# Kernel optimization log

Measured on AMD Instinct MI355X. Metric: run time of the kernel, lower is better.

## Reference

```python
import jax, jax.numpy as jnp
import numpy as np

SR = 22050
FLOOR = 60.0
BPO = 12

def _interp_linear(p, T):
    # torch F.interpolate(mode='linear', align_corners=False)
    S = p.shape[0]
    x = np.clip((np.arange(T, dtype=np.float64) + 0.5) * (S / T) - 0.5, 0.0, S - 1)
    i0 = np.floor(x).astype(np.int64)
    i1 = np.minimum(i0 + 1, S - 1)
    f = (x - i0).astype(np.float32)
    return p[i0] * (1.0 - f) + p[i1] * f

def _hann(n):
    # torch.hann_window(n, periodic=True)
    if n <= 0:
        return np.zeros((0,), np.float32)
    return (0.5 - 0.5 * np.cos(2.0 * np.pi * np.arange(n) / n)).astype(np.float32)

def _find_voiced(f0, i):
    sub = f0[i:]
    if sub.size == 0:
        return None
    flag = (sub > 0.0).astype(np.int64)
    flag[0] = 0
    if not flag.any():
        return None
    rel = int(flag.argmax())
    after = flag[rel:]
    z = np.nonzero(after == 0)[0]
    run = int(z[0]) if z.size else int(after.size)
    return i + rel, i + rel + run

def _l2n(v):
    # F.normalize(dim=-1), eps=1e-12
    return v / np.maximum(np.linalg.norm(v, axis=-1, keepdims=True), 1e-12)

def _find_peak(signal, f0, i, right_dir):
    w = int(SR / max(float(f0[i]), FLOOR))
    s = max(i - w // 2, 0)
    if right_dir:
        cand_l, cand_r = int(i + 0.3 * w), int(i + 0.75 * w)
    else:
        cand_l, cand_r = max(int(i - 1.75 * w), 0), max(int(i - 1.3 * w), 0)
    if cand_l == cand_r or len(signal) - cand_l < w:
        return w, -1.0, i, 0.0
    seg = np.lib.stride_tricks.sliding_window_view(signal[cand_l:cand_r + w], w)
    corr = _l2n(seg) @ _l2n(signal[s:s + w])
    r = int(corr.argmax())
    return w, float(corr[r]), i + (r + cand_l) - s, float(np.abs(seg[r]).max())

def _find_allpeaks(signal, f0):
    gp = float(np.abs(signal).max())
    added_right, i, peaks = -1e308, 0, []
    while True:
        voiced = _find_voiced(f0, i)
        if voiced is None:
            break
        left, right = voiced
        middle = (left + right) // 2
        w = int(SR / float(f0[middle]))
        s = max(middle - w // 2, 0)
        seg = signal[s:s + w]
        mn, imn = float(seg.min()), int(seg.argmin())
        mx, imx = float(seg.max()), int(seg.argmax())
        i = middle if mn == mx else s + (imn if abs(mn) > abs(mx) else imx)
        backup = i
        while True:
            w, corr, i, peak = _find_peak(signal, f0, i, False)
            if corr == -1.0:
                i -= w
            if i < left:
                if corr > 0.7 and peak > 0.023333 * gp and i - added_right > 0.8 * w:
                    peaks.append(i)
                break
            if corr > 0.3 and (peak == 0.0 or peak > 0.01 * gp):
                if i - added_right > 0.8 * w:
                    peaks.append(i)
        i = backup
        while True:
            w, corr, i, peak = _find_peak(signal, f0, i, True)
            if corr == -1.0:
                i += w
            if i >= right:
                if corr > 0.7 and peak > 0.023333 * gp:
                    peaks.append(i)
                    added_right = i
                break
            if corr > 0.3 and (peak == 0.0 or peak > 0.01 * gp):
                peaks.append(i)
                added_right = i
        i = right
    if not peaks:
        return None
    return np.clip(np.array(sorted(peaks), dtype=np.int64), 0, len(signal) - 1)

def _psola_plan(signal, pitch, peaks):
    # Returns list of (dst_idx, src_idx, window) overlap-add ops plus tail index.
    T = len(signal)
    idx = np.arange(T)
    max_w = 1.25 * SR / float(pitch[pitch > 0].min())
    ops, i = [], 0
    while i < T:
        voiced = _find_voiced(pitch, i)
        if voiced is None:
            break
        left_v, right_v = voiced
        if i < left_v:
            ops.append((idx[i:left_v], idx[i:left_v], _hann(left_v - i)))
        while left_v < right_v:
            p = int(np.abs(peaks - left_v).argmin())
            period = int(SR / max(float(pitch[left_v]), FLOOR))
            left_w = right_w = period // 2
            if p > 0 and peaks[p] - peaks[p - 1] <= max_w:
                left_w = min(int(peaks[p] - peaks[p - 1]), left_w)
            if p < len(peaks) - 1 and peaks[p + 1] - peaks[p] <= max_w:
                right_w = min(int(peaks[p + 1] - peaks[p]), right_w)
            left_i = max(int(peaks[p]) - left_w, 0)
            right_i = int(peaks[p]) + right_w
            ival = (right_i - left_i) // 2
            if ival <= 0:  # safety guard; unreachable for speech-range pitch
                break
            win = _hann(ival * 2)
            seglen = min(len(idx[left_v - ival:left_v + ival]), len(idx[left_i:left_i + ival * 2]))
            dst = idx[left_v - ival:left_v - ival + seglen]
            src = idx[left_i:left_i + seglen]
            L = min(len(dst), len(src), seglen)
            ops.append((dst[:L], src[:L], win[:L]))
            left_v += ival * 2
        i = right_v
    return ops, i

def _pitch_shift_plan(snd, pitch, steps, pitch_range):
    if not (pitch > 1e-05).any():
        return None
    f0 = _interp_linear(pitch, len(snd))
    peaks = _find_allpeaks(snd, f0)
    if peaks is None:
        return None
    v = np.sort(pitch[pitch > 0.0])
    median = float(v[(len(v) - 1) // 2])  # torch lower median
    factor = 2.0 ** (steps / BPO)
    f0, median = f0 * factor, median * factor
    f0 = np.where(f0 > 0.0, median + (f0 - median) * pitch_range, 0.0).astype(np.float32)
    return _psola_plan(snd, f0, peaks)

def setup_inputs():
    key = jax.random.key(0)
    T, S = 661500, 3000
    t = np.arange(S)
    base = (170.0 + 40.0 * np.sin(2.0 * np.pi * t / 400.0)).astype(np.float32)
    voiced = (t % 75) >= 15  # alternating unvoiced/voiced runs
    pitch = np.where(voiced, base, 0.0).astype(np.float32)
    f0 = _interp_linear(pitch, T)
    phase = 2.0 * np.pi * np.cumsum(f0.astype(np.float64)) / SR
    noise = np.asarray(jax.random.normal(key, (T,)), np.float32)
    snd = np.where(f0 > 0.0, 0.55 * np.sin(phase) + 0.25 * np.sin(2 * phase) + 0.1 * np.sin(3 * phase), 0.0)
    snd = np.clip(snd + 0.02 * noise, -1.0, 1.0).astype(np.float32)
    return {"snd": jnp.asarray(snd), "pitch": jnp.asarray(pitch), "steps": 3, "pitch_range": jnp.float32(1.0)}

def reference(snd, pitch, steps, pitch_range):
    snd_np = np.asarray(snd, np.float32)
    pitch_np = np.asarray(pitch, np.float32)
    plan = _pitch_shift_plan(snd_np, pitch_np, int(steps), float(pitch_range))
    if plan is None:
        return jnp.asarray(snd_np)
    ops, tail = plan
    out = np.zeros_like(snd_np)
    for dst, src, win in ops:
        out[dst] += win * snd_np[src]
    out[tail:] = snd_np[tail:]
    return jnp.asarray(out)
```

## Files before the change

kernel.cpp:

```cpp
#include <hip/hip_runtime.h>
#include <cfloat>
#include <climits>
#include <math.h>

#define SRATE 22050.0
#define WMAX 512
#define RCAP 128
#define LCR 256
#define RCR 512
#define SCAP 16384
#define OPR 256
#define MSL 3072
#define NTW 256
#define NTM 1024
#define PCAP 8192
#define FCAP 16384
#define PSTG 4096
#define SNDW 15872
#define RPW 136

__global__ __launch_bounds__(256) void kinit_stats(const float* __restrict__ pitch, int S, unsigned* scal) {
  __shared__ int sc[256];
  __shared__ int sa[256];
  int tid = threadIdx.x;
  if (tid < 64) scal[tid] = (tid == 1) ? 0x7f800000u : 0u;
  int c = 0, a = 0;
  for (int j = tid; j < S; j += 256) {
    float v = pitch[j];
    if (v > 0.0f) c++;
    if (v > 1e-05f) a = 1;
  }
  sc[tid] = c; sa[tid] = a; __syncthreads();
  for (int st = 128; st; st >>= 1) {
    if (tid < st) { sc[tid] += sc[tid + st]; sa[tid] |= sa[tid + st]; }
    __syncthreads();
  }
  if (tid == 0) { scal[15] = (unsigned)sc[0]; scal[3] = (unsigned)sa[0]; }
}

__global__ __launch_bounds__(256) void kmedsel(const float* __restrict__ pitch, int S, unsigned* scal) {
  __shared__ float sp[MSL];
  __shared__ unsigned hist[256];
  __shared__ unsigned sprefix, smask;
  __shared__ int srank;
  int tid = threadIdx.x;
  int n = (int)scal[15];
  if (n == 0) return;
  bool lds = (S <= MSL);
  if (lds) { for (int q = tid; q < S; q += 256) sp[q] = pitch[q]; }
  if (tid == 0) { sprefix = 0u; smask = 0u; srank = (n - 1) >> 1; }
  __syncthreads();
  for (int shift = 24; shift >= 0; shift -= 8) {
    hist[tid] = 0u;
    __syncthreads();
    unsigned pfx = sprefix, msk = smask;
    for (int q = tid; q < S; q += 256) {
      float v = lds ? sp[q] : pitch[q];
      if (v > 0.0f) {
        unsigned u = __float_as_uint(v);
        if ((u & msk) == pfx) atomicAdd(&hist[(u >> shift) & 255u], 1u);
      }
    }
    __syncthreads();
    if (tid == 0) {
      int r = srank;
      unsigned b = 0;
      for (;;) { unsigned cc = hist[b]; if (r < (int)cc) break; r -= (int)cc; b++; }
      srank = r;
      sprefix = pfx | (b << shift);
      smask = msk | (0xFFu << shift);
    }
    __syncthreads();
  }
  if (tid == 0) scal[2] = sprefix;
}

__device__ __forceinline__ float interp1(const float* __restrict__ pitch, int S, double r, int t) {
  double x = ((double)t + 0.5) * r - 0.5;
  if (x < 0.0) x = 0.0;
  double sm1 = (double)(S - 1);
  if (x > sm1) x = sm1;
  double fl = floor(x);
  int i0 = (int)fl;
  int i1 = i0 + 1; if (i1 > S - 1) i1 = S - 1;
  float f = (float)(x - fl);
  return __fadd_rn(__fmul_rn(pitch[i0], __fsub_rn(1.0f, f)), __fmul_rn(pitch[i1], f));
}

__global__ __launch_bounds__(256) void kprep(const float* __restrict__ pitch, int S, int T,
                                             const float* __restrict__ snd, unsigned* scal,
                                             const int* __restrict__ steps_p, const float* __restrict__ pr_p,
                                             float* __restrict__ f0, float* __restrict__ f0s,
                                             int* __restrict__ pd, int* __restrict__ w0,
                                             int* s0l, int* e0l, int* s1l, int* e1l) {
  __shared__ float smax[256];
  __shared__ unsigned smin[256];
  float med = __uint_as_float(scal[2]);
  double factor = exp2((double)steps_p[0] / 12.0);
  float fac32 = (float)factor;
  float m32 = (float)((double)med * factor);
  float pr32 = pr_p[0];
  double r = (double)S / (double)T;
  float amax = 0.0f;
  unsigned lmin = 0x7f800000u;
  int stride = gridDim.x * blockDim.x;
  for (int t = blockIdx.x * blockDim.x + threadIdx.x; t < T; t += stride) {
    float v = interp1(pitch, S, r, t);
    f0[t] = v;
    float v1 = __fmul_rn(v, fac32);
    float vs = 0.0f;
    if (v1 > 0.0f) vs = __fadd_rn(m32, __fmul_rn(__fsub_rn(v1, m32), pr32));
    f0s[t] = vs;
    { double fd = (double)vs; if (fd < 60.0) fd = 60.0; pd[t] = (int)(SRATE / fd); }
    { double fi = (double)v; if (fi < 60.0) fi = 60.0;
      int ww = (int)(SRATE / fi); if (ww < 1) ww = 1; if (ww > WMAX - 1) ww = WMAX - 1;
      w0[t] = ww; }
    if (vs > 0.0f) { unsigned b = __float_as_uint(vs); if (b < lmin) lmin = b; }
    float a = fabsf(snd[t]); if (a > amax) amax = a;
    bool pv = false, pv1 = false;
    if (t > 0) {
      float pvv = interp1(pitch, S, r, t - 1);
      pv = pvv > 0.0f;
      float pm1 = __fmul_rn(pvv, fac32);
      float pvs = 0.0f;
      if (pm1 > 0.0f) pvs = __fadd_rn(m32, __fmul_rn(__fsub_rn(pm1, m32), pr32));
      pv1 = pvs > 0.0f;
    }
    bool cv = v > 0.0f, cv1 = vs > 0.0f;
    if (cv && (t == 0 || !pv))  { unsigned k = atomicAdd(scal + 8, 1u);  if (k < RCAP) s0l[k] = t; }
    if (!cv && t > 0 && pv)     { unsigned k = atomicAdd(scal + 9, 1u);  if (k < RCAP) e0l[k] = t; }
    if (cv1 && (t == 0 || !pv1)){ unsigned k = atomicAdd(scal + 10, 1u); if (k < RCAP) s1l[k] = t; }
    if (!cv1 && t > 0 && pv1)   { unsigned k = atomicAdd(scal + 11, 1u); if (k < RCAP) e1l[k] = t; }
  }
  smax[threadIdx.x] = amax; smin[threadIdx.x] = lmin; __syncthreads();
  for (int st = 128; st; st >>= 1) {
    if (threadIdx.x < st) {
      float o = smax[threadIdx.x + st]; if (o > smax[threadIdx.x]) smax[threadIdx.x] = o;
      unsigned u = smin[threadIdx.x + st]; if (u < smin[threadIdx.x]) smin[threadIdx.x] = u;
    }
    __syncthreads();
  }
  if (threadIdx.x == 0) {
    atomicMax(scal + 0, __float_as_uint(smax[0]));
    atomicMin(scal + 1, smin[0]);
  }
}

__device__ void ranksort(int* a, int n, int tid, int* tmp) {
  int v = 0, rk = 0;
  if (tid < n) {
    v = a[tid];
    for (int q = 0; q < n; q++) if (a[q] < v) rk++;
  }
  __syncthreads();
  if (tid < n) tmp[rk] = v;
  __syncthreads();
  if (tid < n) a[tid] = tmp[tid];
  __syncthreads();
}

__device__ int pair_regions_lds(float f1, int T, int* sl, int ns, int* el, int ne, int* L, int* R) {
  int b = 0;
  if (ns > 0 && sl[0] == 0) {
    if (T > 1 && f1 > 0.0f) sl[0] = 1;
    else b = 1;
  }
  int m = 0, j = 0;
  for (int k = b; k < ns; k++) {
    int Lv = sl[k];
    while (j < ne && el[j] <= Lv) j++;
    int Rv = (j < ne) ? el[j] : T;
    if (m < RCAP) { L[m] = Lv; R[m] = Rv; m++; }
  }
  return m;
}

__global__ __launch_bounds__(128) void kregsort2(const float* __restrict__ f0, const float* __restrict__ f0s,
                                                 int T, unsigned* scal,
                                                 const int* __restrict__ s0l, const int* __restrict__ e0l,
                                                 const int* __restrict__ s1l, const int* __restrict__ e1l,
                                                 int* r0L, int* r0R, int* r1L, int* r1R) {
  __shared__ int A[RCAP], B[RCAP], C[RCAP], D[RCAP];
  __shared__ int tmp[RCAP];
  __shared__ int LA[RCAP], RA[RCAP];
  int tid = threadIdx.x;
  int ns0 = min((int)scal[8], RCAP), ne0 = min((int)scal[9], RCAP);
  int ns1 = min((int)scal[10], RCAP), ne1 = min((int)scal[11], RCAP);
  if (tid < ns0) A[tid] = s0l[tid];
  if (tid < ne0) B[tid] = e0l[tid];
  if (tid < ns1) C[tid] = s1l[tid];
  if (tid < ne1) D[tid] = e1l[tid];
  __syncthreads();
  ranksort(A, ns0, tid, tmp);
  ranksort(B, ne0, tid, tmp);
  ranksort(C, ns1, tid, tmp);
  ranksort(D, ne1, tid, tmp);
  float f0_1 = (T > 1) ? f0[1] : 0.0f;
  float f0s_1 = (T > 1) ? f0s[1] : 0.0f;
  __shared__ int m0s, m1s;
  if (tid == 0) {
    m0s = pair_regions_lds(f0_1, T, A, ns0, B, ne0, LA, RA);
  }
  __syncthreads();
  if (tid < m0s) { r0L[tid] = LA[tid]; r0R[tid] = RA[tid]; }
  __syncthreads();
  if (tid == 0) {
    m1s = pair_regions_lds(f0s_1, T, C, ns1, D, ne1, LA, RA);
  }
  __syncthreads();
  if (tid < m1s) { r1L[tid] = LA[tid]; r1R[tid] = RA[tid]; }
  if (tid == 0) { scal[12] = (unsigned)m0s; scal[13] = (unsigned)m1s; }
}

struct FPRes { int w; int i; float corr; float peak; };
struct FPG { int w, s, cl, nw, rlen; bool ok; };

__device__ __forceinline__ FPG fp_geom(int T, int i, int w, bool right_dir) {
  FPG g;
  int s = i - w / 2; if (s < 0) s = 0;
  int cl, cr;
  if (right_dir) {
    cl = (int)((double)i + 0.3 * (double)w);
    cr = (int)((double)i + 0.75 * (double)w);
  } else {
    double al = (double)i - 1.75 * (double)w;
    double bl = (double)i - 1.3 * (double)w;
    cl = (int)al; if (cl < 0) cl = 0;
    cr = (int)bl; if (cr < 0) cr = 0;
  }
  g.w = w; g.s = s; g.cl = cl;
  g.ok = !(cl == cr || T - cl < w);
  int nw = (((cr + w) < T ? (cr + w) : T)) - cl - w + 1;
  if (nw < 1) nw = 1;
  g.nw = nw;
  int rlen = T - s; if (rlen > w) rlen = w;
  g.rlen = rlen;
  return g;
}

template <bool L>
__device__ __forceinline__ FPRes fp_impl(const float* __restrict__ snd, const float* lsnd, int wb0,
                                         FPG g, int i, int tid,
                                         float (*refp)[RPW], double* sdd, float* swf, int* swi, float* swp) {
  FPRes res;
  int w = g.w, s = g.s, cl = g.cl, nw = g.nw, rlen = g.rlen;
  res.w = w;
  int lane = tid & 63, wv = tid >> 6;
  double part = 0.0;
  for (int k = tid; k < w; k += NTW) {
    float v = (k < rlen) ? (L ? lsnd[s + k - wb0] : snd[s + k]) : 0.0f;
    refp[k & 3][k >> 2] = v;
    part += (double)v * (double)v;
  }
  for (int off = 32; off; off >>= 1) part += __shfl_xor(part, off, 64);
  if (lane == 0) sdd[wv] = part;
  __syncthreads();
  double refden = sqrt(sdd[0] + sdd[1] + sdd[2] + sdd[3]);
  if (refden < 1e-12) refden = 1e-12;
  int gg = tid >> 2, sub = tid & 3;
  float bestv = -FLT_MAX; int bestr = INT_MAX; float bestp = 0.0f;
  for (int base = 0; base < nw; base += 64) {
    int r = base + gg;
    if (r < nw) {
      const float* seg = (L ? (lsnd + (cl - wb0)) : (snd + cl)) + r;
      const float* rrow = refp[sub];
      double d0 = 0.0, d1 = 0.0, n0 = 0.0, n1 = 0.0;
      float pkc = 0.0f;
      int k = sub, j = 0;
      for (; k + 12 < w; k += 16, j += 4) {
        float4 rv = *reinterpret_cast<const float4*>(rrow + j);
        float a0f = seg[k], a1f = seg[k + 4];
        pkc = fmaxf(pkc, fabsf(a0f));
        pkc = fmaxf(pkc, fabsf(a1f));
        double a0 = (double)a0f, a1 = (double)a1f;
        d0 += a0 * (double)rv.x; n0 += a0 * a0;
        d1 += a1 * (double)rv.y; n1 += a1 * a1;
        float a2f = seg[k + 8], a3f = seg[k + 12];
        pkc = fmaxf(pkc, fabsf(a2f));
        pkc = fmaxf(pkc, fabsf(a3f));
        double a2 = (double)a2f, a3 = (double)a3f;
        d0 += a2 * (double)rv.z; n0 += a2 * a2;
        d1 += a3 * (double)rv.w; n1 += a3 * a3;
      }
      for (; k + 4 < w; k += 8) {
        float a0f = seg[k], a1f = seg[k + 4];
        pkc = fmaxf(pkc, fabsf(a0f));
        pkc = fmaxf(pkc, fabsf(a1f));
        double a0 = (double)a0f, b0 = (double)refp[k & 3][k >> 2];
        double a1 = (double)a1f, b1 = (double)refp[(k + 4) & 3][(k + 4) >> 2];
        d0 += a0 * b0; n0 += a0 * a0;
        d1 += a1 * b1; n1 += a1 * a1;
      }
      for (; k < w; k += 4) {
        float af = seg[k];
        pkc = fmaxf(pkc, fabsf(af));
        double a = (double)af; d0 += a * (double)refp[k & 3][k >> 2]; n0 += a * a;
      }
      double dot = d0 + d1, nr2 = n0 + n1;
      dot += __shfl_xor(dot, 1, 64); nr2 += __shfl_xor(nr2, 1, 64);
      pkc = fmaxf(pkc, __shfl_xor(pkc, 1, 64));
      dot += __shfl_xor(dot, 2, 64); nr2 += __shfl_xor(nr2, 2, 64);
      pkc = fmaxf(pkc, __shfl_xor(pkc, 2, 64));
      if (sub == 0) {
        double den = sqrt(nr2); if (den < 1e-12) den = 1e-12;
        float c = (float)(dot / (den * refden));
        if (c > bestv) { bestv = c; bestr = r; bestp = pkc; }
      }
    }
  }
  for (int off = 32; off >= 4; off >>= 1) {
    float ov = __shfl_xor(bestv, off, 64);
    int orr = __shfl_xor(bestr, off, 64);
    float op = __shfl_xor(bestp, off, 64);
    if (ov > bestv || (ov == bestv && orr < bestr)) { bestv = ov; bestr = orr; bestp = op; }
  }
  if (lane == 0) { swf[wv] = bestv; swi[wv] = bestr; swp[wv] = bestp; }
  __syncthreads();
  float bv = swf[0]; int br = swi[0]; float bp = swp[0];
  for (int q = 1; q < 4; q++) {
    float ov = swf[q]; int orr = swi[q]; float op = swp[q];
    if (ov > bv || (ov == bv && orr < br)) { bv = ov; br = orr; bp = op; }
  }
  res.corr = bv;
  res.i = i + (br + cl) - s;
  res.peak = bp;
  return res;
}

__device__ __forceinline__ FPRes find_peak_block(const float* __restrict__ snd,
                                                 const float* lsnd, int wb0, int wb1, bool useW,
                                                 int T, int i, int wcur, bool right_dir, int tid,
                                                 float (*refp)[RPW], double* sdd,
                                                 float* swf, int* swi, float* swp) {
  FPG g = fp_geom(T, i, wcur, right_dir);
  if (!g.ok) { FPRes r; r.w = g.w; r.corr = -1.0f; r.i = i; r.peak = 0.0f; return r; }
  int lo_a = g.s < g.cl ? g.s : g.cl;
  int hi1 = g.s + g.w, hi2 = g.cl + g.nw + g.w;
  int hi_a = hi1 > hi2 ? hi1 : hi2;
  bool inW = useW && lo_a >= wb0 && hi_a <= wb1;
  if (inW) return fp_impl<true>(snd, lsnd, wb0, g, i, tid, refp, sdd, swf, swi, swp);
  return fp_impl<false>(snd, lsnd, wb0, g, i, tid, refp, sdd, swf, swi, swp);
}

__global__ __launch_bounds__(NTW) void kwalk(const float* __restrict__ snd,
                                             const float* __restrict__ pitch, int S,
                                             const int* __restrict__ w0,
                                             int T, const unsigned* scal,
                                             const int* __restrict__ r0L, const int* __restrict__ r0R,
                                             int2* __restrict__ lcand, int* __restrict__ lcnt,
                                             int* __restrict__ rpk, int* __restrict__ rcnt) {
  __shared__ float lsnd[SNDW];
  __shared__ short swtab[SNDW];
  __shared__ __align__(16) float refp[4][RPW];
  __shared__ double sdd[4];
  __shared__ float swf[8];
  __shared__ int swi[8];
  __shared__ float swp[4];
  __shared__ float spitch[PSTG];
  int tid = threadIdx.x;
  int lane = tid & 63, wv = tid >> 6;
  if (scal[3] == 0u) return;
  bool useL = (S <= PSTG);
  if (useL) { for (int k = tid; k < S; k += NTW) spitch[k] = pitch[k]; }
  __syncthreads();
  double rr = (double)S / (double)T;
  int nreg = (int)scal[12];
  float gp = __uint_as_float(scal[0]);
  for (int wid = blockIdx.x; wid < 2 * nreg; wid += gridDim.x) {
    int r = wid >> 1;
    bool rightdir = (wid & 1) != 0;
    int left = r0L[r], right = r0R[r];
    int middle = (left + right) >> 1;
    int wb0 = left - 1024; if (wb0 < 0) wb0 = 0;
    int wb1 = right + 1024; if (wb1 > T) wb1 = T;
    bool useW = (wb1 - wb0) <= SNDW;
    __syncthreads();
    if (useW) {
      for (int k = tid; k < wb1 - wb0; k += NTW) {
        lsnd[k] = snd[wb0 + k];
        swtab[k] = (short)w0[wb0 + k];
      }
    }
    __syncthreads();
    double fm = useL ? (double)interp1(spitch, S, rr, middle) : (double)interp1(pitch, S, rr, middle);
    double wd = SRATE / fm;
    long long wcap = 2LL * (long long)T;
    int w = (wd >= (double)wcap) ? (int)wcap : (int)wd;
    if (w < 1) w = 1;
    int s0 = middle - w / 2; if (s0 < 0) s0 = 0;
    int wlen = w; if (wlen > T - s0) wlen = T - s0;
    float lmn = FLT_MAX; int lmni = INT_MAX;
    float lmx = -FLT_MAX; int lmxi = INT_MAX;
    for (int k = tid; k < wlen; k += NTW) {
      int idx = s0 + k;
      float v = (useW && idx >= wb0 && idx < wb1) ? lsnd[idx - wb0] : snd[idx];
      if (v < lmn) { lmn = v; lmni = k; }
      if (v > lmx) { lmx = v; lmxi = k; }
    }
    for (int off = 32; off; off >>= 1) {
      float ov = __shfl_xor(lmn, off, 64); int oi = __shfl_xor(lmni, off, 64);
      if (ov < lmn || (ov == lmn && oi < lmni)) { lmn = ov; lmni = oi; }
      float ov2 = __shfl_xor(lmx, off, 64); int oi2 = __shfl_xor(lmxi, off, 64);
      if (ov2 > lmx || (ov2 == lmx && oi2 < lmxi)) { lmx = ov2; lmxi = oi2; }
    }
    if (lane == 0) { swf[wv] = lmn; swi[wv] = lmni; swf[4 + wv] = lmx; swi[4 + wv] = lmxi; }
    __syncthreads();
    float mn = swf[0]; int imn = swi[0];
    float mx = swf[4]; int imx = swi[4];
    for (int q = 1; q < 4; q++) {
      float ov = swf[q]; int oi = swi[q];
      if (ov < mn || (ov == mn && oi < imn)) { mn = ov; imn = oi; }
      float ov2 = swf[4 + q]; int oi2 = swi[4 + q];
      if (ov2 > mx || (ov2 == mx && oi2 < imx)) { mx = ov2; imx = oi2; }
    }
    __syncthreads();
    int i;
    if (mn == mx) i = middle;
    else i = s0 + ((fabsf(mn) > fabsf(mx)) ? imn : imx);
    if (!rightdir) {
      int nl = 0, guard = 0;
      for (;;) {
        if (++guard > 500000) break;
        int wcur;
        if (useW && i >= wb0 && i < wb1) wcur = (int)swtab[i - wb0];
        else {
          double fi = useL ? (double)interp1(spitch, S, rr, i) : (double)interp1(pitch, S, rr, i);
          if (fi < 60.0) fi = 60.0;
          int ww = (int)(SRATE / fi); if (ww < 1) ww = 1; if (ww > WMAX - 1) ww = WMAX - 1;
          wcur = ww;
        }
        FPRes p = find_peak_block(snd, lsnd, wb0, wb1, useW, T, i, wcur, false, tid,
                                  refp, sdd, swf, swi, swp);
        i = p.i;
        if (p.corr == -1.0f) i -= p.w;
        if (i < left) {
          if ((double)p.corr > 0.7 && (double)p.peak > 0.023333 * (double)gp) {
            if (nl < LCR) { if (tid == 0) lcand[r * LCR + nl] = make_int2(i, p.w); nl++; }
          }
          break;
        }
        if ((double)p.corr > 0.3 && (p.peak == 0.0f || (double)p.peak > 0.01 * (double)gp)) {
          if (nl < LCR) { if (tid == 0) lcand[r * LCR + nl] = make_int2(i, p.w); nl++; }
        }
      }
      if (tid == 0) lcnt[r] = nl;
    } else {
      int nr = 0, guard = 0;
      for (;;) {
        if (++guard > 500000) break;
        int wcur;
        if (useW && i >= wb0 && i < wb1) wcur = (int)swtab[i - wb0];
        else {
          double fi = useL ? (double)interp1(spitch, S, rr, i) : (double)interp1(pitch, S, rr, i);
          if (fi < 60.0) fi = 60.0;
          int ww = (int)(SRATE / fi); if (ww < 1) ww = 1; if (ww > WMAX - 1) ww = WMAX - 1;
          wcur = ww;
        }
        FPRes p = find_peak_block(snd, lsnd, wb0, wb1, useW, T, i, wcur, true, tid,
                                  refp, sdd, swf, swi, swp);
        i = p.i;
        if (p.corr == -1.0f) i += p.w;
        if (i >= right) {
          if ((double)p.corr > 0.7 && (double)p.peak > 0.023333 * (double)gp) {
            if (nr < RCR) { if (tid == 0) rpk[r * RCR + nr] = i; nr++; }
          }
          break;
        }
        if ((double)p.corr > 0.3 && (p.peak == 0.0f || (double)p.peak > 0.01 * (double)gp)) {
          if (nr < RCR) { if (tid == 0) rpk[r * RCR + nr] = i; nr++; }
        }
      }
      if (tid == 0) rcnt[r] = nr;
    }
  }
}

__global__ __launch_bounds__(NTM) void kmerge(int T, unsigned* scal,
                                              const int2* __restrict__ lcand, const int* __restrict__ lcnt,
                                              const int* __restrict__ rpk, const int* __restrict__ rcnt,
                                              int* __restrict__ peaks) {
  __shared__ long long arR[RCAP];
  __shared__ long long lastR[RCAP];
  __shared__ int rcs[RCAP];
  __shared__ int lcs[RCAP];
  __shared__ int klc[RCAP];
  __shared__ int off[RCAP + 1];
  __shared__ int sbuf[SCAP];
  __shared__ int unsorted;
  int tid = threadIdx.x;
  int nreg = (int)scal[12];
  if (scal[3] == 0u || nreg == 0) { if (tid == 0) scal[4] = 0u; return; }
  if (tid < nreg) {
    int rc = rcnt[tid];
    rcs[tid] = rc;
    lcs[tid] = lcnt[tid];
    lastR[tid] = (rc > 0) ? (long long)rpk[tid * RCR + rc - 1] : LLONG_MIN;
  }
  __syncthreads();
  if (tid == 0) {
    long long ar = -(1LL << 62);
    for (int r = 0; r < nreg; r++) { arR[r] = ar; if (rcs[r] > 0) ar = lastR[r]; }
  }
  __syncthreads();
  if (tid < nreg) {
    int r = tid, n = lcs[r], c = 0;
    long long ar = arR[r];
    for (int j = 0; j < n; j++) {
      int2 cd = lcand[r * LCR + j];
      if ((double)((long long)cd.x - ar) > 0.8 * (double)cd.y) c++;
    }
    klc[r] = c;
  }
  __syncthreads();
  if (tid == 0) {
    int acc = 0;
    for (int r = 0; r < nreg; r++) { off[r] = acc; acc += klc[r] + rcs[r]; if (acc > SCAP) acc = SCAP; }
    off[nreg] = acc;
    scal[4] = (unsigned)acc;
    unsorted = 0;
  }
  __syncthreads();
  if (tid < nreg) {
    int r = tid;
    long long ar = arR[r];
    int n = lcs[r], pos = off[r];
    for (int j = n - 1; j >= 0; j--) {
      int2 cd = lcand[r * LCR + j];
      if ((double)((long long)cd.x - ar) > 0.8 * (double)cd.y) { if (pos < SCAP) peaks[pos] = cd.x; pos++; }
    }
    int rc = rcs[r];
    for (int j = 0; j < rc; j++) { if (pos < SCAP) peaks[pos] = rpk[r * RCR + j]; pos++; }
  }
  __syncthreads();
  int npk = off[nreg];
  if (npk > 1) {
    for (int k = tid; k < npk - 1; k += NTM) {
      if (peaks[k] > peaks[k + 1]) unsorted = 1;
    }
    __syncthreads();
    if (unsorted) {
      int n2 = 1; while (n2 < npk) n2 <<= 1;
      for (int k = tid; k < n2; k += NTM) sbuf[k] = (k < npk) ? peaks[k] : INT_MAX;
      __syncthreads();
      for (int kk = 2; kk <= n2; kk <<= 1) {
        for (int j = kk >> 1; j > 0; j >>= 1) {
          for (int idx = tid; idx < n2; idx += NTM) {
            int ixj = idx ^ j;
            if (ixj > idx) {
              int a = sbuf[idx], b = sbuf[ixj];
              bool up = ((idx & kk) == 0);
              if ((up && a > b) || (!up && a < b)) { sbuf[idx] = b; sbuf[ixj] = a; }
            }
          }
          __syncthreads();
        }
      }
      for (int k = tid; k < npk; k += NTM) peaks[k] = sbuf[k];
      __syncthreads();
    }
  }
  for (int k = tid; k < npk; k += NTM) { int v = peaks[k]; if (v < 0) v = 0; if (v > T - 1) v = T - 1; peaks[k] = v; }
}

__global__ __launch_bounds__(256) void kplan(const int* __restrict__ pd, int T, unsigned* scal,
                                             const int* __restrict__ peaks,
                                             const int* __restrict__ r1L, const int* __restrict__ r1R,
                                             int4* __restrict__ ops, int* __restrict__ opcnt) {
  __shared__ int sp[PCAP];
  __shared__ int ib[FCAP];
  int tid = threadIdx.x;
  int npk = (int)scal[4];
  int nreg = (int)scal[13];
  int r = (int)blockIdx.x;
  if (scal[3] == 0u || npk == 0) {
    if (r == 0 && tid == 0) { scal[6] = 0u; scal[14] = 0u; }
    return;
  }
  if (r == 0 && tid == 0) {
    scal[6] = (nreg > 0) ? (unsigned)r1R[nreg - 1] : 0u;
    scal[14] = (unsigned)nreg;
  }
  if (r >= nreg) return;
  int prev_right = (r == 0) ? 0 : r1R[r - 1];
  int left_v = r1L[r], right_v = r1R[r];
  int pl_n = npk < PCAP ? npk : PCAP;
  for (int k = tid; k < pl_n; k += 256) sp[k] = peaks[k];
  int span = right_v - left_v;
  int fl_n = span < FCAP ? span : FCAP;
  for (int k = tid; k < fl_n; k += 256) ib[k] = pd[left_v + k];
  __syncthreads();
  if (tid != 0) return;

  auto PRD = [&](int idx) -> int { return (idx < pl_n) ? sp[idx] : peaks[idx]; };

  double minpos = (double)__uint_as_float(scal[1]);
  double max_w = 1.25 * SRATE / minpos;
  int c = 0;
  if (prev_right < left_v) {
    ops[r * OPR + c] = make_int4(prev_right, prev_right, left_v - prev_right, left_v - prev_right);
    c++;
  }
  int lv = left_v, guard = 0;
  int lo = -1;
  int Pm2 = 0, Pm1 = 0, P0 = 0, P1 = 0;
  while (lv < right_v) {
    if (++guard > 500000) break;
    int fo = lv - left_v;
    int period = (fo < fl_n) ? ib[fo] : pd[lv];
    int x = lv;
    if (lo < 0) {
      int a = 0, b = npk;
      while (a < b) { int m = (a + b) >> 1; if (PRD(m) < x) a = m + 1; else b = m; }
      lo = a;
      Pm2 = (lo - 2 >= 0) ? PRD(lo - 2) : 0;
      Pm1 = (lo - 1 >= 0) ? PRD(lo - 1) : 0;
      P0  = (lo < npk) ? PRD(lo) : 0;
      P1  = (lo + 1 < npk) ? PRD(lo + 1) : 0;
    } else {
      while (lo < npk && P0 < x) {
        lo++;
        Pm2 = Pm1; Pm1 = P0; P0 = P1;
        P1 = (lo + 1 < npk) ? PRD(lo + 1) : 0;
      }
    }
    long long d0 = (lo > 0) ? (long long)x - (long long)Pm1 : LLONG_MAX;
    long long d1 = (lo < npk) ? (long long)P0 - (long long)x : LLONG_MAX;
    int p, Pp, Ppm1, Pp1;
    if (d0 <= d1) {
      p = lo - 1;
      int tv = Pm1;
      if (p > 0 && Pm2 == tv) {
        while (p > 0 && PRD(p - 1) == tv) p--;
        Pp = tv;
        Ppm1 = (p > 0) ? PRD(p - 1) : 0;
        Pp1 = (p < npk - 1) ? PRD(p + 1) : 0;
      } else {
        Pp = Pm1; Ppm1 = Pm2; Pp1 = P0;
      }
    } else {
      p = lo; Pp = P0; Ppm1 = Pm1; Pp1 = P1;
    }
    int lw = period >> 1, rw = period >> 1;
    if (p > 0) { long long gp_ = (long long)Pp - (long long)Ppm1; if ((double)gp_ <= max_w && gp_ < (long long)lw) lw = (int)gp_; }
    if (p < npk - 1) { long long gp_ = (long long)Pp1 - (long long)Pp; if ((double)gp_ <= max_w && gp_ < (long long)rw) rw = (int)gp_; }
    int left_i = Pp - lw; if (left_i < 0) left_i = 0;
    int right_i = Pp + rw;
    int ival = (right_i - left_i) >> 1;
    if (ival <= 0) break;
    int a0 = lv - ival;
    int len1 = 0;
    if (a0 >= 0) { int e = lv + ival; if (e > T) e = T; len1 = e - a0; if (len1 < 0) len1 = 0; }
    int e2 = left_i + 2 * ival; if (e2 > T) e2 = T;
    int len2 = e2 - left_i; if (len2 < 0) len2 = 0;
    int seglen = len1 < len2 ? len1 : len2;
    int len_dst = (a0 < 0) ? 0 : ((T - a0 < seglen) ? T - a0 : seglen);
    int len_src = (T - left_i < seglen) ? T - left_i : seglen;
    int L = seglen; if (len_dst < L) L = len_dst; if (len_src < L) L = len_src;
    if (L > 0 && c < OPR) { ops[r * OPR + c] = make_int4(a0, left_i, L, 2 * ival); c++; }
    lv += 2 * ival;
  }
  opcnt[r] = c;
}

__global__ __launch_bounds__(256) void kapply(const float* __restrict__ snd, float* __restrict__ out,
                                              const unsigned* scal, const int4* __restrict__ ops,
                                              const int* __restrict__ opcnt) {
  int nreg = (int)scal[14];
  int total = nreg * OPR;
  for (int slot = blockIdx.x; slot < total; slot += gridDim.x) {
    int r = slot / OPR, j = slot - r * OPR;
    if (j >= opcnt[r]) continue;
    int4 o = ops[r * OPR + j];
    double nn = (double)o.w;
    for (int k = threadIdx.x; k < o.z; k += blockDim.x) {
      double cph = (6.283185307179586 * (double)k) / nn;
      float wv = (float)(0.5 - 0.5 * cos(cph));
      atomicAdd(out + o.x + k, __fmul_rn(wv, snd[o.y + k]));
    }
  }
}

__global__ __launch_bounds__(256) void ktail(const float* __restrict__ snd, float* __restrict__ out,
                                             const unsigned* scal, int T) {
  int tail = (int)scal[6];
  int stride = gridDim.x * blockDim.x;
  for (int t = blockIdx.x * blockDim.x + threadIdx.x; t < T; t += stride)
    if (t >= tail) out[t] = snd[t];
}

extern "C" void kernel_launch(void* const* d_in, const int* in_sizes, int n_in,
                              void* d_out, int out_size, void* d_ws, size_t ws_size,
                              hipStream_t stream) {
  (void)n_in; (void)ws_size;
  int T = in_sizes[0];
  int S = in_sizes[1];
  const float* snd = (const float*)d_in[0];
  const float* pitch = (const float*)d_in[1];
  const int* steps = (const int*)d_in[2];
  const float* prange = (const float*)d_in[3];
  float* out = (float*)d_out;

  char* base = (char*)d_ws;
  size_t off = 0;
  auto alloc = [&](size_t bytes, size_t align) -> char* {
    off = (off + align - 1) & ~(align - 1);
    char* p = base + off;
    off += bytes;
    return p;
  };
  float* f0  = (float*)alloc((size_t)T * 4, 16);
  float* f0s = (float*)alloc((size_t)T * 4, 16);
  int* pd    = (int*)alloc((size_t)T * 4, 16);
  int* w0    = (int*)alloc((size_t)T * 4, 16);
  unsigned* scal = (unsigned*)alloc(256, 16);
  int* s0l = (int*)alloc(RCAP * 4, 4);
  int* e0l = (int*)alloc(RCAP * 4, 4);
  int* s1l = (int*)alloc(RCAP * 4, 4);
  int* e1l = (int*)alloc(RCAP * 4, 4);
  int* r0L = (int*)alloc(RCAP * 4, 4);
  int* r0R = (int*)alloc(RCAP * 4, 4);
  int* r1L = (int*)alloc(RCAP * 4, 4);
  int* r1R = (int*)alloc(RCAP * 4, 4);
  int* lcnt = (int*)alloc(RCAP * 4, 4);
  int* rcnt = (int*)alloc(RCAP * 4, 4);
  int* opcnt = (int*)alloc(RCAP * 4, 4);
  int2* lcand = (int2*)alloc((size_t)RCAP * LCR * 8, 8);
  int* rpk = (int*)alloc((size_t)RCAP * RCR * 4, 4);
  int* peaks = (int*)alloc((size_t)SCAP * 4, 4);
  int4* ops = (int4*)alloc((size_t)RCAP * OPR * 16, 16);

  hipMemsetAsync(d_out, 0, (size_t)out_size * sizeof(float), stream);
  kinit_stats<<<1, 256, 0, stream>>>(pitch, S, scal);
  kmedsel<<<1, 256, 0, stream>>>(pitch, S, scal);
  kprep<<<1024, 256, 0, stream>>>(pitch, S, T, snd, scal, steps, prange, f0, f0s, pd, w0, s0l, e0l, s1l, e1l);
  kregsort2<<<1, 128, 0, stream>>>(f0, f0s, T, scal, s0l, e0l, s1l, e1l, r0L, r0R, r1L, r1R);
  kwalk<<<256, NTW, 0, stream>>>(snd, pitch, S, w0, T, scal, r0L, r0R, lcand, lcnt, rpk, rcnt);
  kmerge<<<1, NTM, 0, stream>>>(T, scal, lcand, lcnt, rpk, rcnt, peaks);
  kplan<<<RCAP, 256, 0, stream>>>(pd, T, scal, peaks, r1L, r1R, ops, opcnt);
  kapply<<<2048, 256, 0, stream>>>(snd, out, scal, ops, opcnt);
  ktail<<<1024, 256, 0, stream>>>(snd, out, scal, T);
}
```

Before: 481.3 us.

## Fuse stats and median kernels, wave-parallelize merge compaction, vectorize plan loads

Merges the pitch statistics kernel and the median-select kernel into one launch, and fills the shared pitch copy during the counting pass. Rewrites the per-region candidate count and compaction in kmerge so each wavefront handles a region using ballot and popcount prefix sums instead of one thread looping serially. Vectorizes the shared-memory fills in kplan with int4 loads, which requires 16-byte alignment of the peaks buffer. The intent is to remove a launch and cut serial latency in single-block kernels along the critical path.

Result: faster. 462.4 us (-3.9%).

```diff
diff --git a/kernel.cpp b/kernel.cpp
--- a/kernel.cpp
+++ b/kernel.cpp
@@ -19,35 +19,32 @@
 #define SNDW 15872
 #define RPW 136
 
-__global__ __launch_bounds__(256) void kinit_stats(const float* __restrict__ pitch, int S, unsigned* scal) {
+
+__global__ __launch_bounds__(256) void kstats(const float* __restrict__ pitch, int S, unsigned* scal) {
+  __shared__ float sp[MSL];
   __shared__ int sc[256];
   __shared__ int sa[256];
-  int tid = threadIdx.x;
-  if (tid < 64) scal[tid] = (tid == 1) ? 0x7f800000u : 0u;
-  int c = 0, a = 0;
-  for (int j = tid; j < S; j += 256) {
-    float v = pitch[j];
-    if (v > 0.0f) c++;
-    if (v > 1e-05f) a = 1;
-  }
-  sc[tid] = c; sa[tid] = a; __syncthreads();
-  for (int st = 128; st; st >>= 1) {
-    if (tid < st) { sc[tid] += sc[tid + st]; sa[tid] |= sa[tid + st]; }
-    __syncthreads();
-  }
-  if (tid == 0) { scal[15] = (unsigned)sc[0]; scal[3] = (unsigned)sa[0]; }
-}
-
-__global__ __launch_bounds__(256) void kmedsel(const float* __restrict__ pitch, int S, unsigned* scal) {
-  __shared__ float sp[MSL];
   __shared__ unsigned hist[256];
   __shared__ unsigned sprefix, smask;
   __shared__ int srank;
   int tid = threadIdx.x;
-  int n = (int)scal[15];
+  if (tid < 64) scal[tid] = (tid == 1) ? 0x7f800000u : 0u;
+  bool lds = (S <= MSL);
+  int c = 0, a = 0;
+  for (int j = tid; j < S; j += 256) {
+    float v = pitch[j];
+    if (lds) sp[j] = v;
+    if (v > 0.0f) c++;
+    if (v > 1e-05f) a = 1;
+  }
+  sc[tid] = c; sa[tid] = a; __syncthreads();
+  for (int st = 128; st; st >>= 1) {
+    if (tid < st) { sc[tid] += sc[tid + st]; sa[tid] |= sa[tid + st]; }
+    __syncthreads();
+  }
+  int n = sc[0];
+  if (tid == 0) { scal[15] = (unsigned)n; scal[3] = (unsigned)sa[0]; }
   if (n == 0) return;
-  bool lds = (S <= MSL);
-  if (lds) { for (int q = tid; q < S; q += 256) sp[q] = pitch[q]; }
   if (tid == 0) { sprefix = 0u; smask = 0u; srank = (n - 1) >> 1; }
   __syncthreads();
   for (int shift = 24; shift >= 0; shift -= 8) {
@@ -488,6 +485,7 @@
   __shared__ int sbuf[SCAP];
   __shared__ int unsorted;
   int tid = threadIdx.x;
+  int lane = tid & 63, wv = tid >> 6;
   int nreg = (int)scal[12];
   if (scal[3] == 0u || nreg == 0) { if (tid == 0) scal[4] = 0u; return; }
   if (tid < nreg) {
@@ -502,14 +500,22 @@
     for (int r = 0; r < nreg; r++) { arR[r] = ar; if (rcs[r] > 0) ar = lastR[r]; }
   }
   __syncthreads();
-  if (tid < nreg) {
-    int r = tid, n = lcs[r], c = 0;
+  for (int r = wv; r < nreg; r += 16) {
+    int n = lcs[r];
     long long ar = arR[r];
-    for (int j = 0; j < n; j++) {
-      int2 cd = lcand[r * LCR + j];
-      if ((double)((long long)cd.x - ar) > 0.8 * (double)cd.y) c++;
-    }
-    klc[r] = c;
+    int cnt = 0;
+    for (int base = 0; base < n; base += 64) {
+      int jp = base + lane;
+      bool pred = false;
+      if (jp < n) {
+        int j = n - 1 - jp;
+        int2 cd = lcand[r * LCR + j];
+        pred = ((double)((long long)cd.x - ar) > 0.8 * (double)cd.y);
+      }
+      unsigned long long m = __ballot(pred);
+      cnt += __popcll(m);
+    }
+    if (lane == 0) klc[r] = cnt;
   }
   __syncthreads();
   if (tid == 0) {
@@ -520,16 +526,31 @@
     unsorted = 0;
   }
   __syncthreads();
-  if (tid < nreg) {
-    int r = tid;
+  for (int r = wv; r < nreg; r += 16) {
     long long ar = arR[r];
-    int n = lcs[r], pos = off[r];
-    for (int j = n - 1; j >= 0; j--) {
-      int2 cd = lcand[r * LCR + j];
-      if ((double)((long long)cd.x - ar) > 0.8 * (double)cd.y) { if (pos < SCAP) peaks[pos] = cd.x; pos++; }
+    int n = lcs[r];
+    int pos0 = off[r];
+    for (int base = 0; base < n; base += 64) {
+      int jp = base + lane;
+      bool pred = false; int val = 0;
+      if (jp < n) {
+        int j = n - 1 - jp;
+        int2 cd = lcand[r * LCR + j];
+        if ((double)((long long)cd.x - ar) > 0.8 * (double)cd.y) { pred = true; val = cd.x; }
+      }
+      unsigned long long m = __ballot(pred);
+      if (pred) {
+        int pre = __popcll(m & ((1ull << lane) - 1ull));
+        int pos = pos0 + pre;
+        if (pos < SCAP) peaks[pos] = val;
+      }
+      pos0 += __popcll(m);
     }
     int rc = rcs[r];
-    for (int j = 0; j < rc; j++) { if (pos < SCAP) peaks[pos] = rpk[r * RCR + j]; pos++; }
+    for (int j = lane; j < rc; j += 64) {
+      int pos = pos0 + j;
+      if (pos < SCAP) peaks[pos] = rpk[r * RCR + j];
+    }
   }
   __syncthreads();
   int npk = off[nreg];
@@ -584,10 +605,23 @@
   int prev_right = (r == 0) ? 0 : r1R[r - 1];
   int left_v = r1L[r], right_v = r1R[r];
   int pl_n = npk < PCAP ? npk : PCAP;
-  for (int k = tid; k < pl_n; k += 256) sp[k] = peaks[k];
+  int pl4 = pl_n & ~3;
+  for (int k = tid * 4; k < pl4; k += 1024) {
+    int4 v = *reinterpret_cast<const int4*>(peaks + k);
+    sp[k] = v.x; sp[k + 1] = v.y; sp[k + 2] = v.z; sp[k + 3] = v.w;
+  }
+  for (int k = pl4 + tid; k < pl_n; k += 256) sp[k] = peaks[k];
   int span = right_v - left_v;
   int fl_n = span < FCAP ? span : FCAP;
-  for (int k = tid; k < fl_n; k += 256) ib[k] = pd[left_v + k];
+  const int* srcp = pd + left_v;
+  int head = (4 - (left_v & 3)) & 3; if (head > fl_n) head = fl_n;
+  for (int k = tid; k < head; k += 256) ib[k] = srcp[k];
+  int rem4 = (fl_n - head) & ~3;
+  for (int k = tid * 4; k < rem4; k += 1024) {
+    int4 v = *reinterpret_cast<const int4*>(srcp + head + k);
+    ib[head + k] = v.x; ib[head + k + 1] = v.y; ib[head + k + 2] = v.z; ib[head + k + 3] = v.w;
+  }
+  for (int k = head + rem4 + tid; k < fl_n; k += 256) ib[k] = srcp[k];
   __syncthreads();
   if (tid != 0) return;
 
@@ -726,12 +760,11 @@
   int* opcnt = (int*)alloc(RCAP * 4, 4);
   int2* lcand = (int2*)alloc((size_t)RCAP * LCR * 8, 8);
   int* rpk = (int*)alloc((size_t)RCAP * RCR * 4, 4);
-  int* peaks = (int*)alloc((size_t)SCAP * 4, 4);
+  int* peaks = (int*)alloc((size_t)SCAP * 4, 16);
   int4* ops = (int4*)alloc((size_t)RCAP * OPR * 16, 16);
 
   hipMemsetAsync(d_out, 0, (size_t)out_size * sizeof(float), stream);
-  kinit_stats<<<1, 256, 0, stream>>>(pitch, S, scal);
-  kmedsel<<<1, 256, 0, stream>>>(pitch, S, scal);
+  kstats<<<1, 256, 0, stream>>>(pitch, S, scal);
   kprep<<<1024, 256, 0, stream>>>(pitch, S, T, snd, scal, steps, prange, f0, f0s, pd, w0, s0l, e0l, s1l, e1l);
   kregsort2<<<1, 128, 0, stream>>>(f0, f0s, T, scal, s0l, e0l, s1l, e1l, r0L, r0R, r1L, r1R);
   kwalk<<<256, NTW, 0, stream>>>(snd, pitch, S, w0, T, scal, r0L, r0R, lcand, lcnt, rpk, rcnt);
```
